# Kernel tuning notes

Hardware: AMD Instinct MI355X
Metric: run time of the kernel (lower is better)

The kernel has to match this reference:

```python
import jax, jax.numpy as jnp
import numpy as np
from jax import lax

DILATIONS = [1, 2, 4, 8, 16, 32, 64, 128, 256, 512]
L = len(DILATIONS)
T = 2048          # input_size (== sequence length)
C = 128           # residual channels
COND = 16         # condition vector dim
B = 8


def conv1d(x, w, dilation=1):
    # x: [B, T, Cin], w: [K, Cin, Cout] (WIO), SAME padding like keras Conv1D
    return lax.conv_general_dilated(
        x, w, window_strides=(1,), padding='SAME',
        rhs_dilation=(dilation,), dimension_numbers=('NWC', 'WIO', 'NWC'))


def setup_inputs() -> dict:
    key = jax.random.key(0)
    ks = iter(jax.random.split(key, 32))
    n = lambda shape, s=0.05: jax.random.normal(next(ks), shape, dtype=jnp.float32) * s
    inp = {
        'x': jax.random.normal(next(ks), (B, T, 1), dtype=jnp.float32),
        'condition': jax.random.normal(next(ks), (B, COND), dtype=jnp.float32),
        # input projection Conv1D(128, 1)
        'Wc': n((1, 1, C)), 'bc': jnp.zeros((C,), jnp.float32),
        # per-block dilated gated convs Conv1D(128, 3), stacked over L blocks
        'Wt': n((L, 3, C, C)), 'bt': jnp.zeros((L, C), jnp.float32),
        'Ws': n((L, 3, C, C)), 'bs': jnp.zeros((L, C), jnp.float32),
        # stacked conditioning Dense weights: 128 Dense(cond->T) per branch per block
        # Dense i weight [COND, T]; stacked & transposed -> [L, COND, T, 128]
        'Dt': n((L, COND, T, C)), 'Bt': jnp.zeros((L, T, C), jnp.float32),
        'Ds': n((L, COND, T, C)), 'Bs': jnp.zeros((L, T, C), jnp.float32),
        # skip / residual 1x1 convs
        'Wskip': n((L, 1, C, C)), 'bskip': jnp.zeros((L, C), jnp.float32),
        'Wres': n((L, 1, C, C)), 'bres': jnp.zeros((L, C), jnp.float32),
        # output head
        'W1': n((3, C, 2048)), 'b1': jnp.zeros((2048,), jnp.float32),
        'W2': n((3, 2048, 256)), 'b2': jnp.zeros((256,), jnp.float32),
        'W3': n((1, 256, 1)), 'b3': jnp.zeros((1,), jnp.float32),
    }
    return inp


def reference(x, condition, Wc, bc, Wt, bt, Ws, bs, Dt, Bt, Ds, Bs,
              Wskip, bskip, Wres, bres, W1, b1, W2, b2, W3, b3):
    h = conv1d(x, Wc) + bc  # [B, T, 128]
    skip_sum = jnp.zeros_like(h)
    for l, d in enumerate(DILATIONS):
        # fused equivalent of 128 per-channel Dense layers + concat:
        # trans[b,t,k] = condition[b,:] @ Dense_k.W + Dense_k.b
        tt = jnp.einsum('bc,ctk->btk', condition, Dt[l]) + Bt[l]
        ts = jnp.einsum('bc,ctk->btk', condition, Ds[l]) + Bs[l]
        g = jnp.tanh(conv1d(h, Wt[l], d) + bt[l] + tt) * \
            jax.nn.sigmoid(conv1d(h, Ws[l], d) + bs[l] + ts)
        skip_sum = skip_sum + conv1d(g, Wskip[l]) + bskip[l]
        h = conv1d(g, Wres[l]) + bres[l] + h
    out = jax.nn.relu(conv1d(skip_sum, W1) + b1)  # [B, T, 2048]
    out = jax.nn.relu(conv1d(out, W2) + b2)       # [B, T, 256]
    out = jnp.tanh(conv1d(out, W3) + b3)          # [B, T, 1]
    return out
```

## Files before the change

### kernel.cpp

```cpp
#include <hip/hip_runtime.h>
#include <hip/hip_bf16.h>
#include <math.h>

#define T 2048
#define C 128
#define BATCH 8
#define NLAYER 10

typedef short bf16x8 __attribute__((ext_vector_type(8)));
typedef float f32x4 __attribute__((ext_vector_type(4)));
typedef unsigned short u16x4 __attribute__((ext_vector_type(4)));

__device__ __forceinline__ float sigmoidf_(float x) {
    return 1.f / (1.f + __expf(-x));
}
__device__ __forceinline__ float tanhf_(float x) {
    float a = fabsf(x);
    float e = __expf(-2.f * a);
    float t = (1.f - e) / (1.f + e);
    return copysignf(t, x);
}
__device__ __forceinline__ ushort f2bf(float v) {
    __hip_bfloat16 h = __float2bfloat16(v);
    return *reinterpret_cast<ushort*>(&h);
}
__device__ __forceinline__ float bf2f(ushort u) {
    unsigned int x = ((unsigned int)u) << 16;
    return __uint_as_float(x);
}

__global__ void k_init(const float* __restrict__ x, const float* __restrict__ Wc,
                       const float* __restrict__ bc, float* __restrict__ h32,
                       ushort* __restrict__ hb, float* __restrict__ skip) {
    int i = blockIdx.x * 256 + threadIdx.x;
    int c = i & 127;
    int pos = i >> 7;
    float v = x[pos] * Wc[c] + bc[c];
    h32[i] = v;
    hb[i] = f2bf(v);
    skip[i] = 0.f;
}

__global__ void k_prep_wg(const float* __restrict__ Wt, const float* __restrict__ Ws,
                          ushort* __restrict__ WGb) {
    int n = blockIdx.x;
    int l = blockIdx.y;
    int t = threadIdx.x;
    int j = t >> 7, ci = t & 127;
    const float* src = (n < 128) ? Wt : Ws;
    int col = n & 127;
    WGb[((size_t)(l * 256 + n)) * 384 + t] = f2bf(src[(((size_t)l * 3 + j) * 128 + ci) * 128 + col]);
}
__global__ void k_prep_wr(const float* __restrict__ Wskip, const float* __restrict__ Wres,
                          ushort* __restrict__ WRb) {
    int n = blockIdx.x;
    int l = blockIdx.y;
    int ci = threadIdx.x;
    const float* src = (n < 128) ? Wskip : Wres;
    int col = n & 127;
    WRb[((size_t)(l * 256 + n)) * 128 + ci] = f2bf(src[((size_t)l * 128 + ci) * 128 + col]);
}
template<int KIN>
__global__ void k_prep_w(const float* __restrict__ W, ushort* __restrict__ Wb, int N) {
    int n = blockIdx.x;
    for (int k = threadIdx.x; k < 3 * KIN; k += blockDim.x)
        Wb[(size_t)n * (3 * KIN) + k] = f2bf(W[(size_t)k * N + n]);
}
__global__ void k_f32_to_bf16(const float* __restrict__ in, ushort* __restrict__ out, int n) {
    int i = blockIdx.x * 256 + threadIdx.x;
    if (i < n) out[i] = f2bf(in[i]);
}

__global__ __launch_bounds__(256) void k_cond(
    const float* __restrict__ cond,
    const float* __restrict__ Dt, const float* __restrict__ Bt,
    const float* __restrict__ Ds, const float* __restrict__ Bs,
    const float* __restrict__ bt, const float* __restrict__ bs,
    ushort* __restrict__ z0, int l0)
{
    const int l  = l0 + blockIdx.y;
    const int ll = blockIdx.y;
    const int k4 = (threadIdx.x & 31) * 4;
    const int tq = threadIdx.x >> 5;
    const int t  = blockIdx.x * 8 + tq;

    __shared__ float sc[128];
    if (threadIdx.x < 128) sc[threadIdx.x] = cond[threadIdx.x];
    __syncthreads();

    const f32x4 btv = *(const f32x4*)(bt + l * 128 + k4);
    const f32x4 bsv = *(const f32x4*)(bs + l * 128 + k4);
    const f32x4 Btv = *(const f32x4*)(Bt + ((size_t)l * T + t) * 128 + k4);
    const f32x4 Bsv = *(const f32x4*)(Bs + ((size_t)l * T + t) * 128 + k4);

    f32x4 zt[8], zs[8];
    #pragma unroll
    for (int b = 0; b < 8; ++b) {
        zt[b] = btv + Btv;
        zs[b] = bsv + Bsv;
    }

    const float* dtp = Dt + (((size_t)l * 16) * T + t) * 128 + k4;
    const float* dsp = Ds + (((size_t)l * 16) * T + t) * 128 + k4;
    #pragma unroll
    for (int c = 0; c < 16; ++c) {
        const f32x4 dv = *(const f32x4*)(dtp + (size_t)c * T * 128);
        const f32x4 sv = *(const f32x4*)(dsp + (size_t)c * T * 128);
        #pragma unroll
        for (int b = 0; b < 8; ++b) {
            const float cb = sc[b * 16 + c];
            zt[b] += cb * dv;
            zs[b] += cb * sv;
        }
    }

    #pragma unroll
    for (int b = 0; b < 8; ++b) {
        size_t zb = (((size_t)ll * 8 + b) * T + t) * 256;
        u16x4 pt, ps;
        #pragma unroll
        for (int j = 0; j < 4; ++j) {
            pt[j] = f2bf(zt[b][j]);
            ps[j] = f2bf(zs[b][j]);
        }
        *(u16x4*)(z0 + zb + k4)       = pt;
        *(u16x4*)(z0 + zb + 128 + k4) = ps;
    }
}

__global__ __launch_bounds__(256) void k_gate(
    const float* __restrict__ h32_in, float* __restrict__ h32_out,
    const ushort* __restrict__ hb_in, ushort* __restrict__ hb_out,
    float* __restrict__ skip32,
    const ushort* __restrict__ WG,
    const ushort* __restrict__ WR,
    const ushort* __restrict__ z0l,
    const float* __restrict__ bskip, const float* __restrict__ bres,
    int d)
{
    __shared__ ushort lds[3 * 32 * 136];
    const int tid  = threadIdx.x;
    const int lane = tid & 63, ln16 = lane & 15, quad = lane >> 4;
    const int wave = tid >> 6;
    const int n_off = wave * 64;
    const int t0 = blockIdx.x * 4;

    #pragma unroll
    for (int it = 0; it < 6; ++it) {
        int task = tid + it * 256;
        int part = task & 15;
        int r = (task >> 4) & 31;
        int j = task >> 9;
        int t = t0 + (r >> 3) + (j - 1) * d;
        int b = r & 7;
        uint4 v = make_uint4(0u, 0u, 0u, 0u);
        if (t >= 0 && t < T) v = *(const uint4*)(hb_in + ((size_t)b * T + t) * 128 + part * 8);
        *(uint4*)(&lds[(j * 32 + r) * 136 + part * 8]) = v;
    }
    __syncthreads();

    f32x4 acc[2][4];
    #pragma unroll
    for (int mt = 0; mt < 2; ++mt)
        #pragma unroll
        for (int nt = 0; nt < 4; ++nt)
            acc[mt][nt] = (f32x4){0.f, 0.f, 0.f, 0.f};

    #pragma unroll
    for (int j = 0; j < 3; ++j) {
        #pragma unroll
        for (int kc = 0; kc < 4; ++kc) {
            bf16x8 af[2], bfr[4];
            #pragma unroll
            for (int mt = 0; mt < 2; ++mt)
                af[mt] = *(const bf16x8*)(&lds[(j * 32 + mt * 16 + ln16) * 136 + kc * 32 + quad * 8]);
            #pragma unroll
            for (int nt = 0; nt < 4; ++nt)
                bfr[nt] = *(const bf16x8*)(WG + (size_t)(n_off + nt * 16 + ln16) * 384 + j * 128 + kc * 32 + quad * 8);
            #pragma unroll
            for (int mt = 0; mt < 2; ++mt)
                #pragma unroll
                for (int nt = 0; nt < 4; ++nt)
                    acc[mt][nt] = __builtin_amdgcn_mfma_f32_16x16x32_bf16(af[mt], bfr[nt], acc[mt][nt], 0, 0, 0);
        }
    }
    __syncthreads();

    #pragma unroll
    for (int mt = 0; mt < 2; ++mt) {
        #pragma unroll
        for (int nt = 0; nt < 4; ++nt) {
            int n = n_off + nt * 16 + ln16;
            #pragma unroll
            for (int r4 = 0; r4 < 4; ++r4) {
                int row = mt * 16 + quad * 4 + r4;
                int b = row & 7, p = row >> 3;
                float z = acc[mt][nt][r4] + bf2f(z0l[((size_t)b * T + t0 + p) * 256 + n]);
                lds[row * 264 + n] = f2bf(z);
            }
        }
    }
    __syncthreads();

    {
        int r = tid >> 3;
        int k0 = (tid & 7) * 16;
        #pragma unroll
        for (int kk = 0; kk < 16; ++kk) {
            int k = k0 + kk;
            float zt = bf2f(lds[r * 264 + k]);
            float zs = bf2f(lds[r * 264 + 128 + k]);
            lds[8704 + r * 136 + k] = f2bf(tanhf_(zt) * sigmoidf_(zs));
        }
    }
    __syncthreads();

    f32x4 acc2[2][4];
    #pragma unroll
    for (int mt = 0; mt < 2; ++mt)
        #pragma unroll
        for (int nt = 0; nt < 4; ++nt)
            acc2[mt][nt] = (f32x4){0.f, 0.f, 0.f, 0.f};

    #pragma unroll
    for (int kc = 0; kc < 4; ++kc) {
        bf16x8 af[2], bfr[4];
        #pragma unroll
        for (int mt = 0; mt < 2; ++mt)
            af[mt] = *(const bf16x8*)(&lds[8704 + (mt * 16 + ln16) * 136 + kc * 32 + quad * 8]);
        #pragma unroll
        for (int nt = 0; nt < 4; ++nt)
            bfr[nt] = *(const bf16x8*)(WR + (size_t)(n_off + nt * 16 + ln16) * 128 + kc * 32 + quad * 8);
        #pragma unroll
        for (int mt = 0; mt < 2; ++mt)
            #pragma unroll
            for (int nt = 0; nt < 4; ++nt)
                acc2[mt][nt] = __builtin_amdgcn_mfma_f32_16x16x32_bf16(af[mt], bfr[nt], acc2[mt][nt], 0, 0, 0);
    }

    #pragma unroll
    for (int mt = 0; mt < 2; ++mt) {
        #pragma unroll
        for (int nt = 0; nt < 4; ++nt) {
            int n = n_off + nt * 16 + ln16;
            int k = n & 127;
            #pragma unroll
            for (int r4 = 0; r4 < 4; ++r4) {
                int row = mt * 16 + quad * 4 + r4;
                int b = row & 7, p = row >> 3;
                size_t idx = ((size_t)b * T + t0 + p) * 128 + k;
                float v = acc2[mt][nt][r4];
                if (n < 128) {
                    skip32[idx] += v + bskip[k];
                } else {
                    float hv = v + bres[k] + h32_in[idx];
                    h32_out[idx] = hv;
                    hb_out[idx] = f2bf(hv);
                }
            }
        }
    }
}

template<int KIN, bool OUT_BF16>
__global__ __launch_bounds__(256) void k_conv_mfma(
    const ushort* __restrict__ A, const ushort* __restrict__ Wb,
    const float* __restrict__ bias, void* __restrict__ outv,
    int b_in_off, int b_out_off)
{
    constexpr int AS = 40;
    __shared__ ushort As[66 * AS];
    __shared__ ushort Bs[3 * 128 * AS];

    const int tid  = threadIdx.x;
    const int lane = tid & 63;
    const int ln16 = lane & 15;
    const int quad = lane >> 4;
    const int wave = tid >> 6;
    const int m_off = (wave & 1) * 32;
    const int n_off = (wave >> 1) * 64;

    const int t0 = blockIdx.x * 64;
    const int n0 = blockIdx.y * 128;
    const int bz = blockIdx.z;
    const int N  = gridDim.y * 128;

    const ushort* Ab = A + (size_t)(b_in_off + bz) * T * KIN;

    f32x4 acc[2][4];
    #pragma unroll
    for (int mi = 0; mi < 2; ++mi)
        #pragma unroll
        for (int ni = 0; ni < 4; ++ni)
            acc[mi][ni] = (f32x4){0.f, 0.f, 0.f, 0.f};

    for (int cc = 0; cc < KIN / 32; ++cc) {
        for (int idx = tid; idx < 66 * 4; idx += 256) {
            int r = idx >> 2, part = idx & 3;
            int t = t0 - 1 + r;
            uint4 v = make_uint4(0u, 0u, 0u, 0u);
            if (t >= 0 && t < T)
                v = *(const uint4*)(Ab + (size_t)t * KIN + cc * 32 + part * 8);
            *(uint4*)(&As[r * AS + part * 8]) = v;
        }
        #pragma unroll
        for (int it = 0; it < 6; ++it) {
            int idx = tid + it * 256;
            int jr = idx >> 2, part = idx & 3;
            int j = jr >> 7, n = jr & 127;
            uint4 v = *(const uint4*)(Wb + (size_t)(n0 + n) * (3 * KIN) + j * KIN + cc * 32 + part * 8);
            *(uint4*)(&Bs[jr * AS + part * 8]) = v;
        }
        __syncthreads();

        #pragma unroll
        for (int j = 0; j < 3; ++j) {
            bf16x8 af[2], bf[4];
            #pragma unroll
            for (int mi = 0; mi < 2; ++mi)
                af[mi] = *(const bf16x8*)(&As[(m_off + mi * 16 + ln16 + j) * AS + quad * 8]);
            #pragma unroll
            for (int ni = 0; ni < 4; ++ni)
                bf[ni] = *(const bf16x8*)(&Bs[(j * 128 + n_off + ni * 16 + ln16) * AS + quad * 8]);
            #pragma unroll
            for (int mi = 0; mi < 2; ++mi)
                #pragma unroll
                for (int ni = 0; ni < 4; ++ni)
                    acc[mi][ni] = __builtin_amdgcn_mfma_f32_16x16x32_bf16(af[mi], bf[ni], acc[mi][ni], 0, 0, 0);
        }
        __syncthreads();
    }

    #pragma unroll
    for (int ni = 0; ni < 4; ++ni) {
        int n = n0 + n_off + ni * 16 + ln16;
        float bv = bias[n];
        #pragma unroll
        for (int mi = 0; mi < 2; ++mi) {
            #pragma unroll
            for (int r = 0; r < 4; ++r) {
                int m = m_off + mi * 16 + quad * 4 + r;
                int t = t0 + m;
                float v = fmaxf(acc[mi][ni][r] + bv, 0.f);
                size_t oi = ((size_t)(b_out_off + bz) * T + t) * N + n;
                if constexpr (OUT_BF16) ((ushort*)outv)[oi] = f2bf(v);
                else                    ((float*)outv)[oi]  = v;
            }
        }
    }
}

__global__ __launch_bounds__(256) void k_conv3(
    const float* __restrict__ out2, const float* __restrict__ W3,
    const float* __restrict__ b3, float* __restrict__ out)
{
    int wid = threadIdx.x >> 6, lane = threadIdx.x & 63;
    int pos = blockIdx.x * 4 + wid;
    float4 v = *(const float4*)(out2 + (size_t)pos * 256 + lane * 4);
    float4 w = *(const float4*)(W3 + lane * 4);
    float sum = v.x * w.x + v.y * w.y + v.z * w.z + v.w * w.w;
    #pragma unroll
    for (int off = 32; off > 0; off >>= 1) sum += __shfl_down(sum, off);
    if (lane == 0) out[pos] = tanhf_(sum + b3[0]);
}

extern "C" void kernel_launch(void* const* d_in, const int* in_sizes, int n_in,
                              void* d_out, int out_size, void* d_ws, size_t ws_size,
                              hipStream_t stream)
{
    const float* x     = (const float*)d_in[0];
    const float* cond  = (const float*)d_in[1];
    const float* Wc    = (const float*)d_in[2];
    const float* bc    = (const float*)d_in[3];
    const float* Wt    = (const float*)d_in[4];
    const float* bt    = (const float*)d_in[5];
    const float* Ws    = (const float*)d_in[6];
    const float* bs    = (const float*)d_in[7];
    const float* Dt    = (const float*)d_in[8];
    const float* Bt    = (const float*)d_in[9];
    const float* Ds    = (const float*)d_in[10];
    const float* Bs    = (const float*)d_in[11];
    const float* Wskip = (const float*)d_in[12];
    const float* bskip = (const float*)d_in[13];
    const float* Wres  = (const float*)d_in[14];
    const float* bres  = (const float*)d_in[15];
    const float* W1    = (const float*)d_in[16];
    const float* b1    = (const float*)d_in[17];
    const float* W2    = (const float*)d_in[18];
    const float* b2    = (const float*)d_in[19];
    const float* W3    = (const float*)d_in[20];
    const float* b3    = (const float*)d_in[21];
    float* out = (float*)d_out;

    float* ws = (float*)d_ws;
    float*  skip32 = ws;
    float*  h32a   = ws + 2097152;
    float*  h32b   = ws + 4194304;
    float*  out2   = ws + 6291456;
    ushort* u      = (ushort*)(ws + 10485760);
    ushort* hba    = u;
    ushort* hbb    = u + 2097152;
    ushort* WGb    = u + 4194304;
    ushort* WRb    = u + 5177344;
    ushort* W1b    = u + 5505024;
    ushort* W2b    = u + 6291456;
    ushort* skipb  = u + 7864320;
    ushort* z0     = u + 9961472;
    ushort* out1b  = z0;

    int nb = 8;
    while (nb > 1) {
        size_t need = 41943040ull + 2ull * (9961472ull + (size_t)nb * 4194304ull);
        if (need <= ws_size) break;
        nb >>= 1;
    }

    k_init<<<8192, 256, 0, stream>>>(x, Wc, bc, h32a, hba, skip32);
    k_prep_wg<<<dim3(256, NLAYER), 384, 0, stream>>>(Wt, Ws, WGb);
    k_prep_wr<<<dim3(256, NLAYER), 128, 0, stream>>>(Wskip, Wres, WRb);
    k_prep_w<128><<<2048, 384, 0, stream>>>(W1, W1b, 2048);
    k_prep_w<2048><<<256, 1024, 0, stream>>>(W2, W2b, 256);

    static const int DIL[NLAYER] = {1, 2, 4, 8, 16, 32, 64, 128, 256, 512};
    float*  h32in = h32a;  float*  h32out = h32b;
    ushort* hbin  = hba;   ushort* hbout  = hbb;

    for (int chunk = 0; chunk < 2; ++chunk) {
        int l0 = chunk * 5;
        k_cond<<<dim3(T / 8, 5), 256, 0, stream>>>(cond, Dt, Bt, Ds, Bs, bt, bs, z0, l0);
        for (int l = l0; l < l0 + 5; ++l) {
            k_gate<<<512, 256, 0, stream>>>(
                h32in, h32out, hbin, hbout, skip32,
                WGb + (size_t)l * 256 * 384,
                WRb + (size_t)l * 256 * 128,
                z0 + (size_t)(l - l0) * 8 * T * 256,
                bskip + l * 128, bres + l * 128,
                DIL[l]);
            float* tf = h32in; h32in = h32out; h32out = tf;
            ushort* tu = hbin; hbin = hbout; hbout = tu;
        }
    }

    k_f32_to_bf16<<<(BATCH * T * C + 255) / 256, 256, 0, stream>>>(skip32, skipb, BATCH * T * C);

    for (int b0 = 0; b0 < BATCH; b0 += nb) {
        int nbc = (b0 + nb <= BATCH) ? nb : (BATCH - b0);
        k_conv_mfma<128, true><<<dim3(T / 64, 16, nbc), 256, 0, stream>>>(skipb, W1b, b1, out1b, b0, 0);
        k_conv_mfma<2048, false><<<dim3(T / 64, 2, nbc), 256, 0, stream>>>(out1b, W2b, b2, out2, 0, b0);
    }

    k_conv3<<<(BATCH * T) / 4, 256, 0, stream>>>(out2, W3, b3, out);
}
```

Baseline: 910.1 us.

## Add dedicated double-buffered MFMA kernel for the 2048->256 head conv

Replaces the generic conv kernel for the second head conv with a new kernel using 128x128 tiles, direct global-to-LDS loads, XOR-swizzled shared memory and double buffering over 64-wide K chunks. The intermediate activations are written into a zero-padded buffer (T+2 rows per batch) so the kernel needs no boundary handling, and the batch-chunking loop is removed so all batches run in one launch. The aim is better reuse and latency hiding in the dominant GEMM-like conv. The grid is only 256 blocks and each needs about 133KB of LDS, which may limit occupancy on the device.

```diff
diff --git a/kernel.cpp b/kernel.cpp
--- a/kernel.cpp
+++ b/kernel.cpp
@@ -27,6 +27,11 @@
 __device__ __forceinline__ float bf2f(ushort u) {
     unsigned int x = ((unsigned int)u) << 16;
     return __uint_as_float(x);
+}
+__device__ __forceinline__ void gl_lds16(const ushort* g, ushort* l) {
+    __builtin_amdgcn_global_load_lds(
+        (const __attribute__((address_space(1))) unsigned int*)g,
+        (__attribute__((address_space(3))) unsigned int*)l, 16, 0, 0);
 }
 
 __global__ void k_init(const float* __restrict__ x, const float* __restrict__ Wc,
@@ -69,6 +74,12 @@
 __global__ void k_f32_to_bf16(const float* __restrict__ in, ushort* __restrict__ out, int n) {
     int i = blockIdx.x * 256 + threadIdx.x;
     if (i < n) out[i] = f2bf(in[i]);
+}
+__global__ void k_zero_pad(ushort* __restrict__ out1p) {
+    int i = blockIdx.x * 256 + threadIdx.x;
+    int ri = i >> 10, col = i & 1023;
+    int b = ri >> 1, pr = (ri & 1) ? 2049 : 0;
+    ((unsigned int*)out1p)[((size_t)b * 2050 + pr) * 1024 + col] = 0u;
 }
 
 __global__ __launch_bounds__(256) void k_cond(
@@ -266,7 +277,7 @@
 __global__ __launch_bounds__(256) void k_conv_mfma(
     const ushort* __restrict__ A, const ushort* __restrict__ Wb,
     const float* __restrict__ bias, void* __restrict__ outv,
-    int b_in_off, int b_out_off)
+    int b_in_off, int b_out_off, int ots, int oto)
 {
     constexpr int AS = 40;
     __shared__ ushort As[66 * AS];
@@ -342,9 +353,111 @@
                 int m = m_off + mi * 16 + quad * 4 + r;
                 int t = t0 + m;
                 float v = fmaxf(acc[mi][ni][r] + bv, 0.f);
-                size_t oi = ((size_t)(b_out_off + bz) * T + t) * N + n;
+                size_t oi = ((size_t)(b_out_off + bz) * ots + oto + t) * N + n;
                 if constexpr (OUT_BF16) ((ushort*)outv)[oi] = f2bf(v);
                 else                    ((float*)outv)[oi]  = v;
+            }
+        }
+    }
+}
+
+#define CV2_AUS 8704
+#define CV2_BUS 24576
+#define CV2_BUF 33280
+
+__global__ __launch_bounds__(256) void k_conv2t(
+    const ushort* __restrict__ A,
+    const ushort* __restrict__ Wb,
+    const float* __restrict__ bias,
+    float* __restrict__ out2)
+{
+    __shared__ ushort sh[2 * CV2_BUF];
+    const int tid  = threadIdx.x;
+    const int lane = tid & 63, ln16 = lane & 15, quad = lane >> 4;
+    const int wave = tid >> 6;
+    const int wm = wave >> 1, wn = wave & 1;
+    const int m0 = blockIdx.x * 128;
+    const int b  = blockIdx.y;
+    const int n0 = blockIdx.z * 128;
+    const size_t aRow0 = (size_t)b * 2050 + m0;
+
+    f32x4 acc[4][4];
+    #pragma unroll
+    for (int i = 0; i < 4; ++i)
+        #pragma unroll
+        for (int j = 0; j < 4; ++j) acc[i][j] = (f32x4){0.f, 0.f, 0.f, 0.f};
+
+    auto stage = [&](int d, int cc) {
+        const int sb = d * CV2_BUF;
+        const int k0 = cc * 64;
+        #pragma unroll
+        for (int ps = 0; ps < 4; ++ps) {
+            int task = ps * 256 + tid;
+            int r = task >> 3, p = task & 7, q = p ^ (r & 7);
+            gl_lds16(A + (aRow0 + r) * 2048 + k0 + q * 8,
+                     &sh[sb + ((ps * 256 + wave * 64) << 3)]);
+        }
+        if (tid < 64) {
+            int task = 1024 + tid;
+            int r = task >> 3, p = task & 7, q = p ^ (r & 7);
+            gl_lds16(A + (aRow0 + r) * 2048 + k0 + q * 8,
+                     &sh[sb + (1024 << 3)]);
+        }
+        #pragma unroll
+        for (int ps = 0; ps < 12; ++ps) {
+            int task = ps * 256 + tid;
+            int rb = task >> 3, p = task & 7, q = p ^ (rb & 7);
+            int nl = rb & 127, tap = rb >> 7;
+            gl_lds16(Wb + (size_t)(n0 + nl) * 6144 + tap * 2048 + k0 + q * 8,
+                     &sh[sb + CV2_AUS + ((ps * 256 + wave * 64) << 3)]);
+        }
+    };
+
+    stage(0, 0);
+    __syncthreads();
+
+    for (int cc = 0; cc < 32; ++cc) {
+        if (cc < 31) stage((cc + 1) & 1, cc + 1);
+        const int sb = (cc & 1) * CV2_BUF;
+        #pragma unroll
+        for (int j = 0; j < 3; ++j) {
+            #pragma unroll
+            for (int kk = 0; kk < 2; ++kk) {
+                bf16x8 af[4], bfr[4];
+                #pragma unroll
+                for (int mt = 0; mt < 4; ++mt) {
+                    int r = wm * 64 + mt * 16 + ln16 + j;
+                    int s = (kk << 2) | quad;
+                    af[mt] = *(const bf16x8*)(&sh[sb + r * 64 + ((s ^ (r & 7)) << 3)]);
+                }
+                #pragma unroll
+                for (int nt = 0; nt < 4; ++nt) {
+                    int rb = j * 128 + wn * 64 + nt * 16 + ln16;
+                    int s = (kk << 2) | quad;
+                    bfr[nt] = *(const bf16x8*)(&sh[sb + CV2_AUS + rb * 64 + ((s ^ (rb & 7)) << 3)]);
+                }
+                #pragma unroll
+                for (int mt = 0; mt < 4; ++mt)
+                    #pragma unroll
+                    for (int nt = 0; nt < 4; ++nt)
+                        acc[mt][nt] = __builtin_amdgcn_mfma_f32_16x16x32_bf16(af[mt], bfr[nt], acc[mt][nt], 0, 0, 0);
+            }
+        }
+        __syncthreads();
+    }
+
+    #pragma unroll
+    for (int nt = 0; nt < 4; ++nt) {
+        int n = n0 + wn * 64 + nt * 16 + ln16;
+        float bv = bias[n];
+        #pragma unroll
+        for (int mt = 0; mt < 4; ++mt) {
+            #pragma unroll
+            for (int r4 = 0; r4 < 4; ++r4) {
+                int m = wm * 64 + mt * 16 + quad * 4 + r4;
+                int t = m0 + m;
+                float v = fmaxf(acc[mt][nt][r4] + bv, 0.f);
+                out2[((size_t)b * T + t) * 256 + n] = v;
             }
         }
     }
@@ -404,16 +517,9 @@
     ushort* WRb    = u + 5177344;
     ushort* W1b    = u + 5505024;
     ushort* W2b    = u + 6291456;
-    ushort* skipb  = u + 7864320;
+    ushort* skipb  = u;
     ushort* z0     = u + 9961472;
-    ushort* out1b  = z0;
-
-    int nb = 8;
-    while (nb > 1) {
-        size_t need = 41943040ull + 2ull * (9961472ull + (size_t)nb * 4194304ull);
-        if (need <= ws_size) break;
-        nb >>= 1;
-    }
+    ushort* out1p  = u + 7864320;
 
     k_init<<<8192, 256, 0, stream>>>(x, Wc, bc, h32a, hba, skip32);
     k_prep_wg<<<dim3(256, NLAYER), 384, 0, stream>>>(Wt, Ws, WGb);
@@ -442,12 +548,9 @@
     }
 
     k_f32_to_bf16<<<(BATCH * T * C + 255) / 256, 256, 0, stream>>>(skip32, skipb, BATCH * T * C);
-
-    for (int b0 = 0; b0 < BATCH; b0 += nb) {
-        int nbc = (b0 + nb <= BATCH) ? nb : (BATCH - b0);
-        k_conv_mfma<128, true><<<dim3(T / 64, 16, nbc), 256, 0, stream>>>(skipb, W1b, b1, out1b, b0, 0);
-        k_conv_mfma<2048, false><<<dim3(T / 64, 2, nbc), 256, 0, stream>>>(out1b, W2b, b2, out2, 0, b0);
-    }
-
+    k_zero_pad<<<64, 256, 0, stream>>>(out1p);
+    k_conv_mfma<128, true><<<dim3(T / 64, 16, BATCH), 256, 0, stream>>>(
+        skipb, W1b, b1, out1p, 0, 0, 2050, 1);
+    k_conv2t<<<dim3(16, 8, 2), 256, 0, stream>>>(out1p, W2b, b2, out2);
     k_conv3<<<(BATCH * T) / 4, 256, 0, stream>>>(out2, W3, b3, out);
 }
```

New measurement: 867.8 us. 1.05x faster.
